# Kernel tuning notes

Measured on AMD Instinct MI355X. Metric: run time of the kernel, lower is better.

The kernel has to match this reference:

```python
import jax, jax.numpy as jnp
import numpy as np

NUM_HEADS = 8


def setup_inputs() -> dict:
    key = jax.random.key(0)
    ks = jax.random.split(key, 6)
    B, C, H, W = 64, 512, 16, 16
    x = jax.random.normal(ks[0], (B, C, H, W), dtype=jnp.float32)
    qkv_w = jax.random.normal(ks[1], (3 * C, C), dtype=jnp.float32) * (C ** -0.5)
    qkv_b = jax.random.normal(ks[2], (3 * C,), dtype=jnp.float32) * 0.02
    out_w = jax.random.normal(ks[3], (C, C), dtype=jnp.float32) * (C ** -0.5)
    out_b = jax.random.normal(ks[4], (C,), dtype=jnp.float32) * 0.02
    rel_pos_enc = jax.random.normal(ks[5], (NUM_HEADS, 2 * 16 - 1, 2 * 16 - 1), dtype=jnp.float32) * 0.02
    return {"x": x, "qkv_w": qkv_w, "qkv_b": qkv_b, "out_w": out_w,
            "out_b": out_b, "rel_pos_enc": rel_pos_enc}


def _attention(x, qkv_w, qkv_b, out_w, out_b, rel_pos_enc):
    B, C, H, W = x.shape
    heads = rel_pos_enc.shape[0]
    hd = C // heads
    N = H * W

    # 1x1 conv qkv projection == pointwise GEMM over channels
    qkv = jnp.einsum('bchw,oc->bohw', x, qkv_w) + qkv_b[None, :, None, None]
    q, k, v = jnp.split(qkv, 3, axis=1)  # each (B, C, H, W)
    q = q.reshape(B, heads, hd, N)
    k = k.reshape(B, heads, hd, N)
    v = v.reshape(B, heads, hd, N)

    attn = jnp.einsum('bhdn,bhdm->bhnm', q, k) * (hd ** -0.5)  # (B,h,N,N)

    # gathered 2D relative position bias: bias[head,(h1,w1),(h2,w2)] =
    #   rel_pos_enc[head, h1-h2+15, w1-w2+15]
    h_idx = (jnp.arange(H)[:, None] - jnp.arange(H)[None, :]) + 16 - 1  # (H,H)
    w_idx = (jnp.arange(W)[:, None] - jnp.arange(W)[None, :]) + 16 - 1  # (W,W)
    bias = rel_pos_enc[:, h_idx[:, None, :, None], w_idx[None, :, None, :]]  # (h,H,W,H,W)
    bias = bias.reshape(heads, N, N)

    attn = jax.nn.softmax(attn + bias[None], axis=-1)
    out = jnp.einsum('bhnm,bhdm->bhdn', attn, v).reshape(B, C, H, W)
    out = jnp.einsum('bchw,oc->bohw', out, out_w) + out_b[None, :, None, None]
    return out


def reference(x, qkv_w, qkv_b, out_w, out_b, rel_pos_enc):
    return _attention(x, qkv_w, qkv_b, out_w, out_b, rel_pos_enc)
```

## Files before the change

kernel.cpp:

```cpp
#include <hip/hip_runtime.h>

typedef __attribute__((ext_vector_type(8))) short short8;
typedef __attribute__((ext_vector_type(4))) float floatx4;
typedef __attribute__((ext_vector_type(4))) int   intx4;

#define MFMA16(a,b,c) __builtin_amdgcn_mfma_f32_16x16x32_bf16((a),(b),(c),0,0,0)

static __device__ __forceinline__ unsigned short f2bf(float f){
    unsigned int u = __float_as_uint(f);
    u = (u + 0x7FFFu + ((u >> 16) & 1u)) >> 16;
    return (unsigned short)u;
}

static __device__ __forceinline__ unsigned int pkbf(float lo, float hi){
    unsigned int r;
    asm("v_cvt_pk_bf16_f32 %0, %1, %2" : "=v"(r) : "v"(lo), "v"(hi));
    return r;
}

static __device__ __forceinline__ void async16(const unsigned short* g, const unsigned short* l){
    __builtin_amdgcn_global_load_lds(
        (const __attribute__((address_space(1))) unsigned int*)g,
        (__attribute__((address_space(3))) unsigned int*)l, 16, 0, 0);
}

__global__ __launch_bounds__(256) void k_prep(const float* __restrict__ x,
                                              unsigned short* __restrict__ xT,
                                              const float* __restrict__ qkvw,
                                              unsigned short* __restrict__ wqkv,
                                              const float* __restrict__ outw,
                                              unsigned short* __restrict__ wout,
                                              const float* __restrict__ rel,
                                              unsigned short* __restrict__ Bp){
    __shared__ unsigned short tile[64][78];
    const int bid = blockIdx.x;
    const int tid = threadIdx.x;
    if (bid < 2048){
        const int c0 = (bid & 7) * 64;
        const int n0 = ((bid >> 3) & 3) * 64;
        const int b  = bid >> 5;
        const int chunk = tid & 7;
        const int r     = tid >> 3;
        const float*    src = x  + (size_t)b * 131072;
        unsigned short* dst = xT + (size_t)b * 131072;
#pragma unroll
        for (int it = 0; it < 2; ++it){
            int c = r + it * 32;
            const float* p = src + (size_t)(c0 + c) * 256 + n0 + chunk * 8;
            float4 f0 = *(const float4*)(p);
            float4 f1 = *(const float4*)(p + 4);
            short8 v;
            v[0]=(short)f2bf(f0.x); v[1]=(short)f2bf(f0.y); v[2]=(short)f2bf(f0.z); v[3]=(short)f2bf(f0.w);
            v[4]=(short)f2bf(f1.x); v[5]=(short)f2bf(f1.y); v[6]=(short)f2bf(f1.z); v[7]=(short)f2bf(f1.w);
            *(short8*)&tile[c][chunk * 8] = v;
        }
        __syncthreads();
#pragma unroll
        for (int it = 0; it < 2; ++it){
            int n = r + it * 32;
            short8 o;
#pragma unroll
            for (int e = 0; e < 8; ++e) o[e] = (short)tile[chunk * 8 + e][n];
            *(short8*)(dst + (size_t)(n0 + n) * 512 + c0 + chunk * 8) = o;
        }
    } else if (bid < 3072){
        int i = (bid - 2048) * 256 + tid;
        const float* s; unsigned short* d; int j;
        if (i < 196608){ s = qkvw; d = wqkv; j = i; }
        else { j = i - 196608; if (j >= 65536) return; s = outw; d = wout; }
        float4 f = *(const float4*)(s + (size_t)j * 4);
        uint2 v;
        v.x = (unsigned int)f2bf(f.x) | ((unsigned int)f2bf(f.y) << 16);
        v.y = (unsigned int)f2bf(f.z) | ((unsigned int)f2bf(f.w) << 16);
        *(uint2*)(d + (size_t)j * 4) = v;
    } else {
        int idx  = (bid - 3072) * 256 + tid;
        int lane = idx & 63;
        int ct   = (idx >> 6) & 15;
        int pp   = (idx >> 10) & 1;
        int wv   = (idx >> 11) & 7;
        int h    = idx >> 14;
        int token = wv * 32 + pp * 16 + (lane & 15);
        int key0  = 32 * (ct >> 1) + 8 * (lane >> 4) + 4 * (ct & 1);
        int th = token >> 4, tw = token & 15;
        int kh = key0 >> 4,  kw0 = key0 & 15;
        int base = h * 961 + (th - kh + 15) * 31 + (tw - kw0 + 15);
        float v0 = rel[base]     * 1.44269504f;
        float v1 = rel[base - 1] * 1.44269504f;
        float v2 = rel[base - 2] * 1.44269504f;
        float v3 = rel[base - 3] * 1.44269504f;
        uint2 o; o.x = pkbf(v0, v1); o.y = pkbf(v2, v3);
        *(uint2*)(Bp + (size_t)idx * 4) = o;
    }
}

__global__ __launch_bounds__(512, 2) void k_fused(const unsigned short* __restrict__ xT,
                                                  const unsigned short* __restrict__ wbf,
                                                  const float* __restrict__ qkvb,
                                                  const unsigned short* __restrict__ Bp,
                                                  unsigned short* __restrict__ ao){
    __shared__ unsigned short SH[77824];
    const int XS = 0;
    const int WS = 16384;
    const int QS = 28672;
    const int KS = 45056;
    const int VS = 61440;

    const int bid  = blockIdx.x;
    const int xcd  = bid & 7;
    const int slot = bid >> 3;
    const int b = xcd * 8 + (slot & 7);
    const int h = slot >> 3;
    const int tid  = threadIdx.x;
    const int wave = tid >> 6;
    const int lane = tid & 63;
    const int lrow = lane & 15;
    const int lgrp = lane >> 4;
    const int mq = wave >> 1;
    const int nh = wave & 1;

    const uint2* bpw = (const uint2*)Bp + (((size_t)h * 8 + wave) * 2) * 1024 + lane;
    uint2 bA[16], bB[16];
#pragma unroll
    for (int ct = 0; ct < 16; ++ct){
        bA[ct] = bpw[ct * 64];
        bB[ct] = bpw[(16 + ct) * 64];
    }

    floatx4 acc[4][6];
#pragma unroll
    for (int i = 0; i < 4; ++i)
#pragma unroll
        for (int j = 0; j < 6; ++j){ floatx4 z = {0.f,0.f,0.f,0.f}; acc[i][j] = z; }

    const unsigned short* xb = xT + (size_t)(b * 256) * 512;
    const unsigned short* xsrc[4]; int xdo[4];
#pragma unroll
    for (int c = 0; c < 4; ++c){
        int s   = (c * 8 + wave) * 64 + lane;
        int row = s >> 3, pch = s & 7;
        int sch = pch ^ (row & 7);
        xsrc[c] = xb + (size_t)row * 512 + sch * 8;
        xdo[c]  = (c * 8 + wave) * 512;
    }
    const unsigned short* wsrc[3]; int wdo[3];
#pragma unroll
    for (int c = 0; c < 3; ++c){
        int s   = (c * 8 + wave) * 64 + lane;
        int row = s >> 3, pch = s & 7;
        int sch = pch ^ (row & 7);
        int grow = (row >> 6) * 512 + h * 64 + (row & 63);
        wsrc[c] = wbf + (size_t)grow * 512 + sch * 8;
        wdo[c]  = (c * 8 + wave) * 512;
    }

    auto stageA = [&](int XBs, int WBs, int kk){
#pragma unroll
        for (int c = 0; c < 4; ++c) async16(xsrc[c] + kk, &SH[XBs + xdo[c]]);
#pragma unroll
        for (int c = 0; c < 3; ++c) async16(wsrc[c] + kk, &SH[WBs + wdo[c]]);
    };
    auto compA = [&](int XBs, int WBs){
#pragma unroll
        for (int ks = 0; ks < 2; ++ks){
            short8 af[4], bq[6];
#pragma unroll
            for (int mt = 0; mt < 4; ++mt){
                int row = mq * 64 + mt * 16 + lrow;
                int pch = (ks * 4 + lgrp) ^ (row & 7);
                af[mt] = *(const short8*)&SH[XBs + row * 64 + pch * 8];
            }
#pragma unroll
            for (int nt = 0; nt < 6; ++nt){
                int row = nh * 96 + nt * 16 + lrow;
                int pch = (ks * 4 + lgrp) ^ (row & 7);
                bq[nt] = *(const short8*)&SH[WBs + row * 64 + pch * 8];
            }
#pragma unroll
            for (int mt = 0; mt < 4; ++mt)
#pragma unroll
                for (int nt = 0; nt < 6; ++nt)
                    acc[mt][nt] = MFMA16(af[mt], bq[nt], acc[mt][nt]);
        }
    };

    stageA(XS, WS, 0);
    stageA(QS, KS, 64);
#pragma unroll
    for (int t2 = 0; t2 < 4; ++t2){
        asm volatile("s_waitcnt vmcnt(7)" ::: "memory");
        __builtin_amdgcn_s_barrier();
        asm volatile("" ::: "memory");
        compA(XS, WS);
        asm volatile("" ::: "memory");
        if (t2 < 3){
            __builtin_amdgcn_s_barrier();
            stageA(XS, WS, t2 * 128 + 128);
            asm volatile("s_waitcnt vmcnt(7)" ::: "memory");
        } else {
            asm volatile("s_waitcnt vmcnt(0)" ::: "memory");
        }
        __builtin_amdgcn_s_barrier();
        asm volatile("" ::: "memory");
        compA(QS, KS);
        asm volatile("" ::: "memory");
        __builtin_amdgcn_s_barrier();
        if (t2 < 3) stageA(QS, KS, t2 * 128 + 192);
    }

#pragma unroll
    for (int mt = 0; mt < 4; ++mt){
#pragma unroll
        for (int nt = 0; nt < 6; ++nt){
            int col = nh * 96 + nt * 16 + lrow;
            int seg = col >> 6, off = col & 63;
            float bv = qkvb[seg * 512 + h * 64 + off];
            int token0 = mq * 64 + mt * 16 + lgrp * 4;
            if (seg == 2){
                int lch = token0 >> 3;
                int pch = (lch & 24) | ((lch & 7) ^ (off & 7));
                uint2 vv;
                vv.x = pkbf(acc[mt][nt][0] + bv, acc[mt][nt][1] + bv);
                vv.y = pkbf(acc[mt][nt][2] + bv, acc[mt][nt][3] + bv);
                *(uint2*)&SH[VS + off * 256 + pch * 8 + (lgrp & 1) * 4] = vv;
            } else if (seg == 1){
#pragma unroll
                for (int r = 0; r < 4; ++r){
                    int token = token0 + r;
                    int kslot = (token & ~0x1C) | ((token & 4) << 2) | ((token & 0x18) >> 1);
                    int pch   = (off >> 3) ^ (kslot & 7);
                    SH[KS + kslot * 64 + pch * 8 + (off & 7)] = f2bf(acc[mt][nt][r] + bv);
                }
            } else {
#pragma unroll
                for (int r = 0; r < 4; ++r){
                    int token = token0 + r;
                    int pch   = (off >> 3) ^ (token & 7);
                    SH[QS + token * 64 + pch * 8 + (off & 7)] =
                        f2bf((acc[mt][nt][r] + bv) * 0.18033688f);
                }
            }
        }
    }
    __syncthreads();

    short8 aq[2][2];
#pragma unroll
    for (int pp = 0; pp < 2; ++pp)
#pragma unroll
        for (int kc = 0; kc < 2; ++kc){
            int row = wave * 32 + pp * 16 + lrow;
            int pch = (kc * 4 + lgrp) ^ (row & 7);
            aq[pp][kc] = *(const short8*)&SH[QS + row * 64 + pch * 8];
        }

    floatx4 st0[16], st1[16];
    __builtin_amdgcn_s_setprio(1);
#pragma unroll
    for (int ct = 0; ct < 16; ++ct){
        int row  = ct * 16 + lrow;
        int pch0 = lgrp ^ (row & 7);
        short8 k0 = *(const short8*)&SH[KS + row * 64 + pch0 * 8];
        short8 k1 = *(const short8*)&SH[KS + row * 64 + (pch0 ^ 4) * 8];
        floatx4 z0, z1;
        z0[0] = __uint_as_float(bA[ct].x << 16);
        z0[1] = __uint_as_float(bA[ct].x & 0xFFFF0000u);
        z0[2] = __uint_as_float(bA[ct].y << 16);
        z0[3] = __uint_as_float(bA[ct].y & 0xFFFF0000u);
        z1[0] = __uint_as_float(bB[ct].x << 16);
        z1[1] = __uint_as_float(bB[ct].x & 0xFFFF0000u);
        z1[2] = __uint_as_float(bB[ct].y << 16);
        z1[3] = __uint_as_float(bB[ct].y & 0xFFFF0000u);
        z0 = MFMA16(k0, aq[0][0], z0);
        z0 = MFMA16(k1, aq[0][1], z0);
        z1 = MFMA16(k0, aq[1][0], z1);
        z1 = MFMA16(k1, aq[1][1], z1);
        st0[ct] = z0; st1[ct] = z1;
    }
    __builtin_amdgcn_s_setprio(0);

    float inv0, inv1;
    {
        float p0=0.f,p1=0.f,p2=0.f,p3=0.f;
#pragma unroll
        for (int ct = 0; ct < 16; ++ct){
            float e0 = __builtin_amdgcn_exp2f(st0[ct][0]); st0[ct][0]=e0; p0+=e0;
            float e1 = __builtin_amdgcn_exp2f(st0[ct][1]); st0[ct][1]=e1; p1+=e1;
            float e2 = __builtin_amdgcn_exp2f(st0[ct][2]); st0[ct][2]=e2; p2+=e2;
            float e3 = __builtin_amdgcn_exp2f(st0[ct][3]); st0[ct][3]=e3; p3+=e3;
        }
        float s = (p0+p1)+(p2+p3);
        s += __shfl_xor(s, 16, 64);
        s += __shfl_xor(s, 32, 64);
        inv0 = 1.f / s;
    }
    {
        float p0=0.f,p1=0.f,p2=0.f,p3=0.f;
#pragma unroll
        for (int ct = 0; ct < 16; ++ct){
            float e0 = __builtin_amdgcn_exp2f(st1[ct][0]); st1[ct][0]=e0; p0+=e0;
            float e1 = __builtin_amdgcn_exp2f(st1[ct][1]); st1[ct][1]=e1; p1+=e1;
            float e2 = __builtin_amdgcn_exp2f(st1[ct][2]); st1[ct][2]=e2; p2+=e2;
            float e3 = __builtin_amdgcn_exp2f(st1[ct][3]); st1[ct][3]=e3; p3+=e3;
        }
        float s = (p0+p1)+(p2+p3);
        s += __shfl_xor(s, 16, 64);
        s += __shfl_xor(s, 32, 64);
        inv1 = 1.f / s;
    }

    intx4 pf0[8], pf1[8];
#pragma unroll
    for (int ms = 0; ms < 8; ++ms){
        intx4 t0_, t1_;
        t0_.x = (int)pkbf(st0[2*ms  ][0], st0[2*ms  ][1]);
        t0_.y = (int)pkbf(st0[2*ms  ][2], st0[2*ms  ][3]);
        t0_.z = (int)pkbf(st0[2*ms+1][0], st0[2*ms+1][1]);
        t0_.w = (int)pkbf(st0[2*ms+1][2], st0[2*ms+1][3]);
        pf0[ms] = t0_;
        t1_.x = (int)pkbf(st1[2*ms  ][0], st1[2*ms  ][1]);
        t1_.y = (int)pkbf(st1[2*ms  ][2], st1[2*ms  ][3]);
        t1_.z = (int)pkbf(st1[2*ms+1][0], st1[2*ms+1][1]);
        t1_.w = (int)pkbf(st1[2*ms+1][2], st1[2*ms+1][3]);
        pf1[ms] = t1_;
    }

    unsigned short* aob = ao + (size_t)(b * 256) * 512 + h * 64;
    const int n0 = wave * 32 + lrow;
    __builtin_amdgcn_s_setprio(1);
#pragma unroll
    for (int dt = 0; dt < 4; ++dt){
        floatx4 a0 = {0.f,0.f,0.f,0.f}, a1 = {0.f,0.f,0.f,0.f};
#pragma unroll
        for (int ms = 0; ms < 8; ++ms){
            int row = dt * 16 + lrow;
            int lch = ms * 4 + lgrp;
            int pch = (lch & 24) | ((lch & 7) ^ (row & 7));
            short8 vb = *(const short8*)&SH[VS + row * 256 + pch * 8];
            a0 = MFMA16(vb, __builtin_bit_cast(short8, pf0[ms]), a0);
            a1 = MFMA16(vb, __builtin_bit_cast(short8, pf1[ms]), a1);
        }
        uint2 o0, o1;
        o0.x = pkbf(a0[0] * inv0, a0[1] * inv0);
        o0.y = pkbf(a0[2] * inv0, a0[3] * inv0);
        *(uint2*)(aob + (size_t)n0 * 512 + dt * 16 + lgrp * 4) = o0;
        o1.x = pkbf(a1[0] * inv1, a1[1] * inv1);
        o1.y = pkbf(a1[2] * inv1, a1[3] * inv1);
        *(uint2*)(aob + (size_t)(n0 + 16) * 512 + dt * 16 + lgrp * 4) = o1;
    }
    __builtin_amdgcn_s_setprio(0);
}

__global__ __launch_bounds__(256, 2) void k_out(const unsigned short* __restrict__ ao,
                                                const unsigned short* __restrict__ wbf,
                                                const float* __restrict__ bias,
                                                float* __restrict__ out){
    __shared__ unsigned short Ash[2][2][128][32];
    __shared__ unsigned short Bsh[2][2][128][32];
    const int bid  = blockIdx.x;
    const int xcd  = bid & 7;
    const int slot = bid >> 3;
    const int t0 = (xcd * 16 + (slot & 15)) * 128;
    const int o0 = (slot >> 4) * 128;
    const int tid  = threadIdx.x;
    const int wave = tid >> 6;
    const int lane = tid & 63;
    const int lrow = lane & 15;
    const int wm   = (wave >> 1) * 64;
    const int wn   = (wave & 1) * 64;
    const int ld_row = wave * 32 + (lane >> 2);
    const int ld_col = (((lane & 3) ^ ((lane >> 3) & 3))) * 8;
    const int pcho = (((lane >> 4) ^ ((lrow >> 1) & 3))) * 8;

    floatx4 acc[4][4];
#pragma unroll
    for (int i = 0; i < 4; ++i)
#pragma unroll
        for (int j = 0; j < 4; ++j){ floatx4 z = {0.f,0.f,0.f,0.f}; acc[i][j] = z; }

    const unsigned short* gA = wbf + (size_t)(o0 + ld_row) * 512 + ld_col;
    const unsigned short* gB = ao  + (size_t)(t0 + ld_row) * 512 + ld_col;

    auto stage = [&](int d, int kk){
        async16(gA + kk,                 &Ash[d][0][wave * 32][0]);
        async16(gA + kk + 16 * 512,      &Ash[d][0][wave * 32 + 16][0]);
        async16(gA + kk + 32,            &Ash[d][1][wave * 32][0]);
        async16(gA + kk + 32 + 16 * 512, &Ash[d][1][wave * 32 + 16][0]);
        async16(gB + kk,                 &Bsh[d][0][wave * 32][0]);
        async16(gB + kk + 16 * 512,      &Bsh[d][0][wave * 32 + 16][0]);
        async16(gB + kk + 32,            &Bsh[d][1][wave * 32][0]);
        async16(gB + kk + 32 + 16 * 512, &Bsh[d][1][wave * 32 + 16][0]);
    };
    auto comp = [&](int d){
#pragma unroll
        for (int s = 0; s < 2; ++s){
            short8 af[4], bq[4];
#pragma unroll
            for (int mt = 0; mt < 4; ++mt) af[mt] = *(const short8*)&Ash[d][s][wm + mt*16 + lrow][pcho];
#pragma unroll
            for (int nt = 0; nt < 4; ++nt) bq[nt] = *(const short8*)&Bsh[d][s][wn + nt*16 + lrow][pcho];
#pragma unroll
            for (int mt = 0; mt < 4; ++mt)
#pragma unroll
                for (int nt = 0; nt < 4; ++nt)
                    acc[mt][nt] = MFMA16(af[mt], bq[nt], acc[mt][nt]);
        }
    };

    stage(0, 0);
    stage(1, 64);
#pragma unroll
    for (int t2 = 0; t2 < 4; ++t2){
        asm volatile("s_waitcnt vmcnt(8)" ::: "memory");
        __builtin_amdgcn_s_barrier();
        asm volatile("" ::: "memory");
        comp(0);
        asm volatile("" ::: "memory");
        if (t2 < 3){
            __builtin_amdgcn_s_barrier();
            stage(0, t2 * 128 + 128);
            asm volatile("s_waitcnt vmcnt(8)" ::: "memory");
        } else {
            asm volatile("s_waitcnt vmcnt(0)" ::: "memory");
        }
        __builtin_amdgcn_s_barrier();
        asm volatile("" ::: "memory");
        comp(1);
        asm volatile("" ::: "memory");
        __builtin_amdgcn_s_barrier();
        if (t2 < 3) stage(1, t2 * 128 + 192);
    }
#pragma unroll
    for (int mt = 0; mt < 4; ++mt){
        int orow0 = o0 + wm + mt*16 + (lane >> 4) * 4;
#pragma unroll
        for (int nt = 0; nt < 4; ++nt){
            int tcol = t0 + wn + nt*16 + lrow;
            int bb = tcol >> 8, nn = tcol & 255;
#pragma unroll
            for (int r = 0; r < 4; ++r){
                float bv = bias[orow0 + r];
                out[(size_t)(bb * 512 + orow0 + r) * 256 + nn] = acc[mt][nt][r] + bv;
            }
        }
    }
}

extern "C" void kernel_launch(void* const* d_in, const int* in_sizes, int n_in,
                              void* d_out, int out_size, void* d_ws, size_t ws_size,
                              hipStream_t stream){
    const float* x    = (const float*)d_in[0];
    const float* qkvw = (const float*)d_in[1];
    const float* qkvb = (const float*)d_in[2];
    const float* outw = (const float*)d_in[3];
    const float* outb = (const float*)d_in[4];
    const float* rel  = (const float*)d_in[5];
    float* out = (float*)d_out;

    const size_t XT_OFF = 0;
    const size_t AO_OFF = 16777216;
    const size_t W_OFF  = 33554432;
    const size_t NEED   = W_OFF + 4194304;
    if (ws_size < NEED) return;

    char* ws = (char*)d_ws;
    unsigned short* xT = (unsigned short*)(ws + XT_OFF);
    unsigned short* ao = (unsigned short*)(ws + AO_OFF);
    unsigned short* wqkv_bf = (unsigned short*)(ws + W_OFF);
    unsigned short* wout_bf = (unsigned short*)(ws + W_OFF + 2097152);
    unsigned short* Bp      = (unsigned short*)(ws + W_OFF + 2621440);

    hipLaunchKernelGGL(k_prep,  dim3(3584), dim3(256), 0, stream,
                       x, xT, qkvw, wqkv_bf, outw, wout_bf, rel, Bp);
    hipLaunchKernelGGL(k_fused, dim3(512),  dim3(512), 0, stream,
                       xT, wqkv_bf, qkvb, Bp, ao);
    hipLaunchKernelGGL(k_out,   dim3(512),  dim3(256), 0, stream,
                       ao, wout_bf, outb, out);
}
```

Measured before the change: 150.6 us.

## Load QKV GEMM A-operand directly from global into registers, double-buffered

In the QKV projection phase, x tiles are no longer staged through LDS. Each wave loads its A fragments straight from global memory into registers, double-buffered across k-steps, while only the weight tiles still go through async LDS copies, reusing the former x buffers as a second weight buffer. The bias-table register preload is moved after the GEMM loop to lower register pressure during the main loop. The aim is to cut LDS traffic and barriers, at the cost of duplicate global reads of x across the two N-half waves, uncoalesced strided loads, and a more fragile vmcnt accounting.

```diff
diff --git a/kernel.cpp b/kernel.cpp
--- a/kernel.cpp
+++ b/kernel.cpp
@@ -119,14 +119,6 @@
     const int mq = wave >> 1;
     const int nh = wave & 1;
 
-    const uint2* bpw = (const uint2*)Bp + (((size_t)h * 8 + wave) * 2) * 1024 + lane;
-    uint2 bA[16], bB[16];
-#pragma unroll
-    for (int ct = 0; ct < 16; ++ct){
-        bA[ct] = bpw[ct * 64];
-        bB[ct] = bpw[(16 + ct) * 64];
-    }
-
     floatx4 acc[4][6];
 #pragma unroll
     for (int i = 0; i < 4; ++i)
@@ -134,15 +126,7 @@
         for (int j = 0; j < 6; ++j){ floatx4 z = {0.f,0.f,0.f,0.f}; acc[i][j] = z; }
 
     const unsigned short* xb = xT + (size_t)(b * 256) * 512;
-    const unsigned short* xsrc[4]; int xdo[4];
-#pragma unroll
-    for (int c = 0; c < 4; ++c){
-        int s   = (c * 8 + wave) * 64 + lane;
-        int row = s >> 3, pch = s & 7;
-        int sch = pch ^ (row & 7);
-        xsrc[c] = xb + (size_t)row * 512 + sch * 8;
-        xdo[c]  = (c * 8 + wave) * 512;
-    }
+
     const unsigned short* wsrc[3]; int wdo[3];
 #pragma unroll
     for (int c = 0; c < 3; ++c){
@@ -154,22 +138,23 @@
         wdo[c]  = (c * 8 + wave) * 512;
     }
 
-    auto stageA = [&](int XBs, int WBs, int kk){
-#pragma unroll
-        for (int c = 0; c < 4; ++c) async16(xsrc[c] + kk, &SH[XBs + xdo[c]]);
+    auto stageW = [&](int WBs, int kk){
 #pragma unroll
         for (int c = 0; c < 3; ++c) async16(wsrc[c] + kk, &SH[WBs + wdo[c]]);
     };
-    auto compA = [&](int XBs, int WBs){
+    short8 afA[2][4], afB[2][4];
+    auto loadA = [&](short8 (&af)[2][4], int kk){
+#pragma unroll
+        for (int ks = 0; ks < 2; ++ks)
+#pragma unroll
+            for (int mt = 0; mt < 4; ++mt)
+                af[ks][mt] = *(const short8*)(xb +
+                    (size_t)(mq * 64 + mt * 16 + lrow) * 512 + kk + (ks * 4 + lgrp) * 8);
+    };
+    auto compA = [&](short8 (&af)[2][4], int WBs){
 #pragma unroll
         for (int ks = 0; ks < 2; ++ks){
-            short8 af[4], bq[6];
-#pragma unroll
-            for (int mt = 0; mt < 4; ++mt){
-                int row = mq * 64 + mt * 16 + lrow;
-                int pch = (ks * 4 + lgrp) ^ (row & 7);
-                af[mt] = *(const short8*)&SH[XBs + row * 64 + pch * 8];
-            }
+            short8 bq[6];
 #pragma unroll
             for (int nt = 0; nt < 6; ++nt){
                 int row = nh * 96 + nt * 16 + lrow;
@@ -180,33 +165,43 @@
             for (int mt = 0; mt < 4; ++mt)
 #pragma unroll
                 for (int nt = 0; nt < 6; ++nt)
-                    acc[mt][nt] = MFMA16(af[mt], bq[nt], acc[mt][nt]);
-        }
-    };
-
-    stageA(XS, WS, 0);
-    stageA(QS, KS, 64);
-#pragma unroll
-    for (int t2 = 0; t2 < 4; ++t2){
-        asm volatile("s_waitcnt vmcnt(7)" ::: "memory");
+                    acc[mt][nt] = MFMA16(af[ks][mt], bq[nt], acc[mt][nt]);
+        }
+    };
+    auto STEP = [&](int tt, short8 (&cur)[2][4], short8 (&nxt)[2][4], int WB){
+        if (tt < 7) loadA(nxt, tt * 64 + 64);
+        if (tt < 7){ asm volatile("s_waitcnt vmcnt(11)" ::: "memory"); }
+        else       { asm volatile("s_waitcnt vmcnt(0)"  ::: "memory"); }
         __builtin_amdgcn_s_barrier();
         asm volatile("" ::: "memory");
-        compA(XS, WS);
-        asm volatile("" ::: "memory");
-        if (t2 < 3){
+        compA(cur, WB);
+        asm volatile("" ::: "memory");
+        if (tt < 6){
             __builtin_amdgcn_s_barrier();
-            stageA(XS, WS, t2 * 128 + 128);
-            asm volatile("s_waitcnt vmcnt(7)" ::: "memory");
-        } else {
-            asm volatile("s_waitcnt vmcnt(0)" ::: "memory");
-        }
-        __builtin_amdgcn_s_barrier();
-        asm volatile("" ::: "memory");
-        compA(QS, KS);
-        asm volatile("" ::: "memory");
-        __builtin_amdgcn_s_barrier();
-        if (t2 < 3) stageA(QS, KS, t2 * 128 + 192);
-    }
+            stageW(WB, tt * 64 + 128);
+        }
+    };
+
+    stageW(WS, 0);
+    stageW(XS, 64);
+    loadA(afA, 0);
+    STEP(0, afA, afB, WS);
+    STEP(1, afB, afA, XS);
+    STEP(2, afA, afB, WS);
+    STEP(3, afB, afA, XS);
+    STEP(4, afA, afB, WS);
+    STEP(5, afB, afA, XS);
+    STEP(6, afA, afB, WS);
+    STEP(7, afB, afA, XS);
+
+    const uint2* bpw = (const uint2*)Bp + (((size_t)h * 8 + wave) * 2) * 1024 + lane;
+    uint2 bA[16], bB[16];
+#pragma unroll
+    for (int ct = 0; ct < 16; ++ct){
+        bA[ct] = bpw[ct * 64];
+        bB[ct] = bpw[(16 + ct) * 64];
+    }
+    asm volatile("" ::: "memory");
 
 #pragma unroll
     for (int mt = 0; mt < 4; ++mt){
```

Result: slower. 166.8 us (+10.8%).
